# Performance work log

Measured on AMD Instinct MI355X. Metric: run time of the kernel, lower is better.

## Reference

```python
import jax, jax.numpy as jnp
import numpy as np


def _dft_mats(N1, N):
    # Symmetric N1xN1 DFT / iDFT matrices and Cooley-Tukey twiddle factors.
    n = np.arange(N1)
    F = np.exp(-2j * np.pi * np.outer(n, n) / N1).astype(np.complex64)
    Finv = np.conj(F)  # inverse DFT matrix (1/N normalization folded into tw)
    tw = (np.exp(-2j * np.pi * np.outer(n, n) / N) / N).astype(np.complex64)
    twinv = np.exp(2j * np.pi * np.outer(n, n) / N).astype(np.complex64)
    return F, Finv, tw, twinv


def setup_inputs() -> dict:
    key = jax.random.key(0)
    ku, kk = jax.random.split(key)
    B, H, N = 128, 128, 1024
    u = jax.random.normal(ku, (B, H, N), dtype=jnp.float32)
    k = jax.random.normal(kk, (H, N), dtype=jnp.float32)
    return {"u": u, "k": k}


def reference(u, k):
    # Four-step (Monarch / Cooley-Tukey) FFT convolution: y = ifft(fft(u) * fft(k)).real
    # decomposed into N1xN1 complex matmuls with twiddle multiplies, matching TKFFTConv.
    B, H, N = u.shape
    N1 = int(round(np.sqrt(N)))
    F, Finv, tw, twinv = map(jnp.asarray, _dft_mats(N1, N))

    # Filter spectrum, reshaped (k2, k1) then transposed -> (H, k1, k2), as in __init__.
    kf = jnp.fft.fft(k, n=N)                              # (H, N) complex64
    kfT = jnp.swapaxes(kf.reshape(H, N1, N1), -1, -2)     # (H, k1, k2)

    x = u.reshape(B, H, N1, N1).astype(jnp.complex64)     # (B, H, n1, n2)
    x = jnp.einsum('kn,bhnm->bhkm', F, x)                 # DFT over n1 -> (k1, n2)
    x = x * tw                                            # twiddle (includes 1/N)
    x = jnp.einsum('bhkn,nl->bhkl', x, F)                 # DFT over n2 -> (k1, k2)
    x = x * kfT[None]                                     # pointwise filter in freq
    x = jnp.einsum('bhkl,ln->bhkn', x, Finv)              # iDFT over k2 -> (k1, n2)
    x = x * twinv                                         # inverse twiddle
    x = jnp.einsum('nk,bhkm->bhnm', Finv, x)              # iDFT over k1 -> (n1, n2)
    return x.real.reshape(B, H, N)
```

## Files before the change

### kernel.cpp

```cpp
#include <hip/hip_runtime.h>
#include <hip/hip_bf16.h>
#include <math.h>

typedef __attribute__((ext_vector_type(8))) short short8;
typedef __attribute__((ext_vector_type(16))) float f32x16;

union U {
    unsigned u[4];
    short8 s;
};

struct FragH {
    U f[2];
};

static __device__ __forceinline__ unsigned short f2bf(float x) {
    __bf16 b = (__bf16)x;
    return __builtin_bit_cast(unsigned short, b);
}
static __device__ __forceinline__ float bf2f(unsigned short h) {
    return __builtin_bit_cast(float, (unsigned)h << 16);
}
static __device__ __forceinline__ unsigned packbf(float a, float b) {
    return (unsigned)f2bf(a) | ((unsigned)f2bf(b) << 16);
}

#define MFMA(A, B, C) __builtin_amdgcn_mfma_f32_32x32x16_bf16((A).s, (B).s, (C), 0, 0, 0)


__global__ __launch_bounds__(256) void fft_tables(float2* tabs, float2* T1, uint4* Ftab) {
    int gid = blockIdx.x * 256 + threadIdx.x;
    if (gid < 1024) {
        int i = gid;
        int r = i >> 5, c = i & 31;
        float s32, c32;
        sincospif((float)((r * c) & 31) / 16.0f, &s32, &c32);
        s32 = -s32;
        tabs[i]        = make_float2(c32,  s32);
        tabs[1024 + i] = make_float2(c32, -s32);
        float sN, cN;
        sincospif((float)(r * c) / 512.0f, &sN, &cN);
        sN = -sN;
        tabs[2048 + i] = make_float2(cN / 1024.0f, sN / 1024.0f);
        tabs[3072 + i] = make_float2(cN, -sN);
        int m = i >> 6, l = i & 63;
        int row = (m & 3) + 8 * (m >> 2) + 4 * (l >> 5);
        int prod = (l & 31) * row;
        float st, ct;
        sincospif((float)prod / 512.0f, &st, &ct);
        T1[i] = make_float2(ct / 1024.0f, -st / 1024.0f);
    }
    if (gid < 1536) {
        int c = gid >> 9;
        int rem = gid & 511;
        int t = rem >> 8;
        int sub = rem & 255;
        int l = sub >> 2;
        int v = sub & 3;
        int k0 = 16 * t + 8 * (l >> 5) + 2 * v;
        int j = l & 31;
        unsigned short sh[2];
        for (int q = 0; q < 2; q++) {
            int k = k0 + q;
            float sa, ca;
            sincospif((float)((k * j) & 31) / 16.0f, &sa, &ca);
            float base = (c == 0) ? ca : ((c == 1) ? -sa : sa);
            sh[q] = f2bf(base);
        }
        ((unsigned*)Ftab)[((c * 2 + t) * 64 + l) * 4 + v] =
            (unsigned)sh[0] | ((unsigned)sh[1] << 16);
    }
}

__global__ __launch_bounds__(256) void kf_kernel(const float* __restrict__ kin,
                                                 const float2* __restrict__ tabs,
                                                 float2* __restrict__ kf_cd) {
    __shared__ float  sx[1024];
    __shared__ float2 sA[1024];
    const int h = blockIdx.x, t = threadIdx.x;
    for (int i = t; i < 1024; i += 256) sx[i] = kin[h * 1024 + i];
    __syncthreads();
    const int r = t >> 3, c0 = (t & 7) << 2;

    float2 acc[4];
    for (int j = 0; j < 4; j++) acc[j] = make_float2(0.f, 0.f);
    #pragma unroll 8
    for (int n1 = 0; n1 < 32; n1++) {
        float2 f = tabs[r * 32 + n1];
        for (int j = 0; j < 4; j++) {
            float xv = sx[n1 * 32 + c0 + j];
            acc[j].x += f.x * xv;
            acc[j].y += f.y * xv;
        }
    }
    for (int j = 0; j < 4; j++) {
        float2 w = tabs[3072 + r * 32 + c0 + j];
        sA[r * 32 + c0 + j] = make_float2(acc[j].x * w.x + acc[j].y * w.y,
                                          acc[j].y * w.x - acc[j].x * w.y);
    }
    __syncthreads();
    for (int j = 0; j < 4; j++) acc[j] = make_float2(0.f, 0.f);
    #pragma unroll 8
    for (int n2 = 0; n2 < 32; n2++) {
        float2 a = sA[r * 32 + n2];
        for (int j = 0; j < 4; j++) {
            float2 f = tabs[n2 * 32 + c0 + j];
            acc[j].x += a.x * f.x - a.y * f.y;
            acc[j].y += a.x * f.y + a.y * f.x;
        }
    }
    for (int j = 0; j < 4; j++) {
        int k2 = c0 + j;
        int m = (k2 & 3) | ((k2 >> 3) << 2);
        int hl = (k2 >> 2) & 1;
        kf_cd[h * 1024 + m * 64 + hl * 32 + r] = acc[j];
    }
}

static __device__ __forceinline__ void convertH(const f32x16& acc, bool hihalf, FragH& out) {
    unsigned P[8];
    #pragma unroll
    for (int j = 0; j < 8; j++) P[j] = packbf(acc[2 * j], acc[2 * j + 1]);
    #pragma unroll
    for (int t = 0; t < 2; t++) {
        unsigned a0 = P[4 * t + 0], a1 = P[4 * t + 1];
        unsigned b0 = P[4 * t + 2], b1 = P[4 * t + 3];
        unsigned a0x = __shfl_xor(a0, 32), a1x = __shfl_xor(a1, 32);
        unsigned b0x = __shfl_xor(b0, 32), b1x = __shfl_xor(b1, 32);
        out.f[t].u[0] = hihalf ? b0x : a0;
        out.f[t].u[1] = hihalf ? b1x : a1;
        out.f[t].u[2] = hihalf ? b0  : a0x;
        out.f[t].u[3] = hihalf ? b1  : a1x;
    }
}

__global__ __launch_bounds__(256, 2) void conv_mfma(const float* __restrict__ u,
                                                    const float2* __restrict__ T1,
                                                    const uint4* __restrict__ Ftab,
                                                    const float2* __restrict__ KF,
                                                    float* __restrict__ out) {
    const int lane = threadIdx.x & 63;
    const int wave = threadIdx.x >> 6;
    const int w = blockIdx.x * 4 + wave;
    const int h = w >> 6;
    const int col = lane & 31;
    const int hl = lane >> 5;
    const bool hihalf = (hl != 0);

    U F[3][2];
    #pragma unroll
    for (int c = 0; c < 3; c++)
        #pragma unroll
        for (int t = 0; t < 2; t++) {
            uint4 raw = Ftab[(c * 2 + t) * 64 + lane];
            F[c][t].u[0] = raw.x; F[c][t].u[1] = raw.y;
            F[c][t].u[2] = raw.z; F[c][t].u[3] = raw.w;
        }
    float2 t1[16], kf[16];
    #pragma unroll
    for (int m = 0; m < 16; m++) {
        t1[m] = T1[m * 64 + lane];
        kf[m] = KF[h * 1024 + m * 64 + lane];
    }

    const f32x16 Z16 = {0,0,0,0,0,0,0,0,0,0,0,0,0,0,0,0};

    U A[2][2];
    #pragma unroll
    for (int i = 0; i < 2; i++) {
        const int b = (w * 2 + i) & 127;
        const float* up = u + ((size_t)(b * 128 + h) << 10);
        #pragma unroll
        for (int t = 0; t < 2; t++) {
            float xv[8];
            #pragma unroll
            for (int e = 0; e < 8; e++)
                xv[e] = up[(16 * t + 8 * hl + e) * 32 + col];
            #pragma unroll
            for (int v = 0; v < 4; v++)
                A[i][t].u[v] = packbf(xv[2 * v], xv[2 * v + 1]);
        }
    }

    #pragma unroll
    for (int i = 0; i < 2; i++) {
        const int b = (w * 2 + i) & 127;

        f32x16 aR = Z16, aI = Z16;
        #pragma unroll
        for (int t = 0; t < 2; t++) {
            aR = MFMA(A[i][t], F[0][t], aR);
            aI = MFMA(A[i][t], F[1][t], aI);
        }
        #pragma unroll
        for (int m = 0; m < 16; m++) {
            float rr = aR[m] * t1[m].x - aI[m] * t1[m].y;
            float ii = aR[m] * t1[m].y + aI[m] * t1[m].x;
            aR[m] = rr; aI[m] = ii;
        }
        FragH Yr, Yi;
        convertH(aR, hihalf, Yr);
        convertH(aI, hihalf, Yi);

        f32x16 bR = Z16, bI = Z16;
        #pragma unroll
        for (int t = 0; t < 2; t++) {
            bR = MFMA(F[0][t], Yr.f[t], bR); bR = MFMA(F[2][t], Yi.f[t], bR);
            bI = MFMA(F[0][t], Yi.f[t], bI); bI = MFMA(F[1][t], Yr.f[t], bI);
        }
        #pragma unroll
        for (int m = 0; m < 16; m++) {
            float rr = bR[m] * kf[m].x - bI[m] * kf[m].y;
            float ii = bR[m] * kf[m].y + bI[m] * kf[m].x;
            bR[m] = rr; bI[m] = ii;
        }
        FragH Zr, Zi;
        convertH(bR, hihalf, Zr);
        convertH(bI, hihalf, Zi);

        aR = Z16; aI = Z16;
        #pragma unroll
        for (int t = 0; t < 2; t++) {
            aR = MFMA(Zr.f[t], F[0][t], aR); aR = MFMA(Zi.f[t], F[1][t], aR);
            aI = MFMA(Zr.f[t], F[2][t], aI); aI = MFMA(Zi.f[t], F[0][t], aI);
        }
        #pragma unroll
        for (int m = 0; m < 16; m++) {
            float rr = 1024.0f * (aR[m] * t1[m].x + aI[m] * t1[m].y);
            float ii = 1024.0f * (aI[m] * t1[m].x - aR[m] * t1[m].y);
            aR[m] = rr; aI[m] = ii;
        }
        FragH Wr, Wi;
        convertH(aR, hihalf, Wr);
        convertH(aI, hihalf, Wi);

        f32x16 yR = Z16;
        #pragma unroll
        for (int t = 0; t < 2; t++) {
            yR = MFMA(F[0][t], Wr.f[t], yR);
            yR = MFMA(F[1][t], Wi.f[t], yR);
        }
        float* op = out + ((size_t)(b * 128 + h) << 10);
        #pragma unroll
        for (int m = 0; m < 16; m++)
            op[((m & 3) + 8 * (m >> 2) + 4 * hl) * 32 + col] = yR[m];
    }
}

extern "C" void kernel_launch(void* const* d_in, const int* in_sizes, int n_in,
                              void* d_out, int out_size, void* d_ws, size_t ws_size,
                              hipStream_t stream) {
    const float* u = (const float*)d_in[0];
    const float* k = (const float*)d_in[1];
    float* out = (float*)d_out;

    float2* tabs  = (float2*)d_ws;
    float2* T1    = (float2*)((char*)d_ws + 32768);
    uint4*  Ftab  = (uint4*)((char*)d_ws + 49152);
    float2* kf_cd = (float2*)((char*)d_ws + 65536);

    fft_tables<<<16, 256, 0, stream>>>(tabs, T1, Ftab);
    kf_kernel<<<128, 256, 0, stream>>>(k, tabs, kf_cd);
    conv_mfma<<<2048, 256, 0, stream>>>(u, T1, Ftab, kf_cd, out);
}
```

Baseline: 50.63 us.

## Stage twiddle/filter tables in LDS, use permlane32 swap, raise occupancy

Moves the per-lane twiddle and filter-spectrum registers into shared memory, filled once per block, and reads them on demand. This frees VGPRs so launch bounds can rise from 2 to 3 blocks per SIMD. The fragment-transpose helper now uses v_permlane32_swap instead of four shuffles plus selects. The 1/N scale moves from the twiddle table into the filter spectrum, which drops the multiply by 1024 in the inverse twiddle. In exchange it adds LDS reads and a block barrier.

Result: slower. 60.57 us (+19.6%).

```diff
diff --git a/kernel.cpp b/kernel.cpp
--- a/kernel.cpp
+++ b/kernel.cpp
@@ -17,9 +17,6 @@
 static __device__ __forceinline__ unsigned short f2bf(float x) {
     __bf16 b = (__bf16)x;
     return __builtin_bit_cast(unsigned short, b);
-}
-static __device__ __forceinline__ float bf2f(unsigned short h) {
-    return __builtin_bit_cast(float, (unsigned)h << 16);
 }
 static __device__ __forceinline__ unsigned packbf(float a, float b) {
     return (unsigned)f2bf(a) | ((unsigned)f2bf(b) << 16);
@@ -48,7 +45,7 @@
         int prod = (l & 31) * row;
         float st, ct;
         sincospif((float)prod / 512.0f, &st, &ct);
-        T1[i] = make_float2(ct / 1024.0f, -st / 1024.0f);
+        T1[i] = make_float2(ct, -st);
     }
     if (gid < 1536) {
         int c = gid >> 9;
@@ -113,39 +110,48 @@
         int k2 = c0 + j;
         int m = (k2 & 3) | ((k2 >> 3) << 2);
         int hl = (k2 >> 2) & 1;
-        kf_cd[h * 1024 + m * 64 + hl * 32 + r] = acc[j];
-    }
-}
-
-static __device__ __forceinline__ void convertH(const f32x16& acc, bool hihalf, FragH& out) {
-    unsigned P[8];
-    #pragma unroll
-    for (int j = 0; j < 8; j++) P[j] = packbf(acc[2 * j], acc[2 * j + 1]);
+        kf_cd[h * 1024 + m * 64 + hl * 32 + r] =
+            make_float2(acc[j].x * (1.0f / 1024.0f), acc[j].y * (1.0f / 1024.0f));
+    }
+}
+
+static __device__ __forceinline__ void convertP(const f32x16& acc, FragH& out) {
     #pragma unroll
     for (int t = 0; t < 2; t++) {
-        unsigned a0 = P[4 * t + 0], a1 = P[4 * t + 1];
-        unsigned b0 = P[4 * t + 2], b1 = P[4 * t + 3];
-        unsigned a0x = __shfl_xor(a0, 32), a1x = __shfl_xor(a1, 32);
-        unsigned b0x = __shfl_xor(b0, 32), b1x = __shfl_xor(b1, 32);
-        out.f[t].u[0] = hihalf ? b0x : a0;
-        out.f[t].u[1] = hihalf ? b1x : a1;
-        out.f[t].u[2] = hihalf ? b0  : a0x;
-        out.f[t].u[3] = hihalf ? b1  : a1x;
-    }
-}
-
-__global__ __launch_bounds__(256, 2) void conv_mfma(const float* __restrict__ u,
+        unsigned a0 = packbf(acc[8 * t + 0], acc[8 * t + 1]);
+        unsigned a1 = packbf(acc[8 * t + 2], acc[8 * t + 3]);
+        unsigned b0 = packbf(acc[8 * t + 4], acc[8 * t + 5]);
+        unsigned b1 = packbf(acc[8 * t + 6], acc[8 * t + 7]);
+        asm("v_permlane32_swap_b32 %0, %1" : "+v"(a0), "+v"(b0));
+        asm("v_permlane32_swap_b32 %0, %1" : "+v"(a1), "+v"(b1));
+        out.f[t].u[0] = a0;
+        out.f[t].u[1] = a1;
+        out.f[t].u[2] = b0;
+        out.f[t].u[3] = b1;
+    }
+}
+
+__global__ __launch_bounds__(256, 3) void conv_mfma(const float* __restrict__ u,
                                                     const float2* __restrict__ T1,
                                                     const uint4* __restrict__ Ftab,
                                                     const float2* __restrict__ KF,
                                                     float* __restrict__ out) {
-    const int lane = threadIdx.x & 63;
-    const int wave = threadIdx.x >> 6;
+    __shared__ float2 sT1[1024];
+    __shared__ float2 sKF[1024];
+
+    const int tid = threadIdx.x;
+    const int lane = tid & 63;
+    const int wave = tid >> 6;
     const int w = blockIdx.x * 4 + wave;
-    const int h = w >> 6;
+    const int h = blockIdx.x >> 4;
     const int col = lane & 31;
     const int hl = lane >> 5;
-    const bool hihalf = (hl != 0);
+
+    for (int i = tid; i < 1024; i += 256) {
+        sT1[i] = T1[i];
+        sKF[i] = KF[h * 1024 + i];
+    }
+    __syncthreads();
 
     U F[3][2];
     #pragma unroll
@@ -156,12 +162,6 @@
             F[c][t].u[0] = raw.x; F[c][t].u[1] = raw.y;
             F[c][t].u[2] = raw.z; F[c][t].u[3] = raw.w;
         }
-    float2 t1[16], kf[16];
-    #pragma unroll
-    for (int m = 0; m < 16; m++) {
-        t1[m] = T1[m * 64 + lane];
-        kf[m] = KF[h * 1024 + m * 64 + lane];
-    }
 
     const f32x16 Z16 = {0,0,0,0,0,0,0,0,0,0,0,0,0,0,0,0};
 
@@ -194,13 +194,14 @@
         }
         #pragma unroll
         for (int m = 0; m < 16; m++) {
-            float rr = aR[m] * t1[m].x - aI[m] * t1[m].y;
-            float ii = aR[m] * t1[m].y + aI[m] * t1[m].x;
+            float2 tm = sT1[m * 64 + lane];
+            float rr = aR[m] * tm.x - aI[m] * tm.y;
+            float ii = aR[m] * tm.y + aI[m] * tm.x;
             aR[m] = rr; aI[m] = ii;
         }
         FragH Yr, Yi;
-        convertH(aR, hihalf, Yr);
-        convertH(aI, hihalf, Yi);
+        convertP(aR, Yr);
+        convertP(aI, Yi);
 
         f32x16 bR = Z16, bI = Z16;
         #pragma unroll
@@ -210,13 +211,14 @@
         }
         #pragma unroll
         for (int m = 0; m < 16; m++) {
-            float rr = bR[m] * kf[m].x - bI[m] * kf[m].y;
-            float ii = bR[m] * kf[m].y + bI[m] * kf[m].x;
+            float2 kv = sKF[m * 64 + lane];
+            float rr = bR[m] * kv.x - bI[m] * kv.y;
+            float ii = bR[m] * kv.y + bI[m] * kv.x;
             bR[m] = rr; bI[m] = ii;
         }
         FragH Zr, Zi;
-        convertH(bR, hihalf, Zr);
-        convertH(bI, hihalf, Zi);
+        convertP(bR, Zr);
+        convertP(bI, Zi);
 
         aR = Z16; aI = Z16;
         #pragma unroll
@@ -226,13 +228,14 @@
         }
         #pragma unroll
         for (int m = 0; m < 16; m++) {
-            float rr = 1024.0f * (aR[m] * t1[m].x + aI[m] * t1[m].y);
-            float ii = 1024.0f * (aI[m] * t1[m].x - aR[m] * t1[m].y);
+            float2 tm = sT1[m * 64 + lane];
+            float rr = aR[m] * tm.x + aI[m] * tm.y;
+            float ii = aI[m] * tm.x - aR[m] * tm.y;
             aR[m] = rr; aI[m] = ii;
         }
         FragH Wr, Wi;
-        convertH(aR, hihalf, Wr);
-        convertH(aI, hihalf, Wi);
+        convertP(aR, Wr);
+        convertP(aI, Wi);
 
         f32x16 yR = Z16;
         #pragma unroll
```
